# Performance work log

Hardware: AMD Instinct MI355X
Metric: run time of the kernel (lower is better)

## Reference

```python
import jax, jax.numpy as jnp
import numpy as np

NODE_DIM = 8
IN_EDGE_DIM = 4
OUT_EDGE_DIM = 4
HID = 16
N_NODES = 100000
N_EDGES = 3200000
LN_EPS = 1e-5


def _layer_norm(h, gamma, beta):
    mu = jnp.mean(h, axis=-1, keepdims=True)
    var = jnp.mean(jnp.square(h - mu), axis=-1, keepdims=True)
    return (h - mu) * jax.lax.rsqrt(var + LN_EPS) * gamma + beta


def setup_inputs() -> dict:
    key = jax.random.key(0)
    ks = jax.random.split(key, 12)
    in_dim = NODE_DIM * 2 + IN_EDGE_DIM  # 20
    x = jax.random.normal(ks[0], (N_NODES, NODE_DIM), dtype=jnp.float32)
    edge_index = jax.random.randint(ks[1], (2, N_EDGES), 0, N_NODES, dtype=jnp.int64)
    edge_attr = jax.random.normal(ks[2], (N_EDGES, IN_EDGE_DIM), dtype=jnp.float32)
    # MLP params (Kaiming-uniform-ish scaling like torch defaults)
    def lin(k, fan_in, fan_out):
        lim = 1.0 / np.sqrt(fan_in)
        kw, kb = jax.random.split(k)
        W = jax.random.uniform(kw, (fan_in, fan_out), minval=-lim, maxval=lim, dtype=jnp.float32)
        b = jax.random.uniform(kb, (fan_out,), minval=-lim, maxval=lim, dtype=jnp.float32)
        return W, b
    W1, b1 = lin(ks[3], in_dim, HID)
    W2, b2 = lin(ks[4], HID, HID)
    W3, b3 = lin(ks[5], HID, OUT_EDGE_DIM)
    g1 = jnp.ones((HID,), jnp.float32); be1 = jnp.zeros((HID,), jnp.float32)
    g2 = jnp.ones((HID,), jnp.float32); be2 = jnp.zeros((HID,), jnp.float32)
    return {"x": x, "edge_index": edge_index, "edge_attr": edge_attr,
            "W1": W1, "b1": b1, "g1": g1, "be1": be1,
            "W2": W2, "b2": b2, "g2": g2, "be2": be2,
            "W3": W3, "b3": b3}


def reference(x, edge_index, edge_attr, W1, b1, g1, be1, W2, b2, g2, be2, W3, b3):
    frm = edge_index[0]
    to = edge_index[1]
    # gather node features for both endpoints, concat with edge features: [E, 2*node_dim+in_edge_dim]
    inpt = jnp.concatenate([x[frm], x[to], edge_attr.astype(jnp.float32)], axis=1)
    h = _layer_norm(jax.nn.relu(inpt @ W1 + b1), g1, be1)
    h = _layer_norm(jax.nn.relu(h @ W2 + b2), g2, be2)
    return h @ W3 + b3  # [E, out_edge_dim]
```

## Files before the change

kernel.cpp:

```cpp
#include <hip/hip_runtime.h>
#include <stdint.h>


using u16 = unsigned short;
using u32 = uint32_t;
typedef float v2f __attribute__((ext_vector_type(2)));
typedef __attribute__((ext_vector_type(4))) float f32x4;
typedef __attribute__((ext_vector_type(8))) short bf16x8;
typedef __attribute__((ext_vector_type(2))) __bf16 bf16x2;

__device__ __forceinline__ v2f v2fma(v2f a, v2f b, v2f c) {
    return __builtin_elementwise_fma(a, b, c);
}
__device__ __forceinline__ v2f v2max0(v2f a) {
    v2f z = {0.f, 0.f};
    return __builtin_elementwise_max(a, z);
}

__device__ __forceinline__ float bf2f(u16 u) { return __uint_as_float(((u32)u) << 16); }
__device__ __forceinline__ float bflo(u32 u) { return __uint_as_float(u << 16); }
__device__ __forceinline__ float bfhi(u32 u) { return __uint_as_float(u & 0xFFFF0000u); }
__device__ __forceinline__ u32 f2bf(float f) {
    u32 u = __float_as_uint(f);
    return (u + 0x7FFFu + ((u >> 16) & 1u)) >> 16;
}
__device__ __forceinline__ u32 pkbf(float a, float b) {
    bf16x2 t;
    t.x = (__bf16)a;
    t.y = (__bf16)b;
    return __builtin_bit_cast(u32, t);
}
__device__ __forceinline__ float ldw(const void* p, int i, bool bf) {
    return bf ? bf2f(((const u16*)p)[i]) : ((const float*)p)[i];
}

#define WB_W1 0
#define WB_B1 320
#define WB_W2 336
#define WB_B2 592
#define WB_W3 608
#define WB_B3 672
#define WB_TOT 704
#define WV_W1 0
#define WV_B1 160
#define WV_W2 168
#define WV_B2 296
#define WV_W3 304
#define WV_B3 336
#define FQ_A1 0
#define FQ_A2H 512
#define FQ_A2L 1024
#define FQ_A3H 1536
#define FQ_A3L 2048
#define FB_OFF (WB_TOT + 1280)

__global__ __launch_bounds__(256)
void probe_convert(const int* __restrict__ ei, int n_pairs,
                   const void* W1, const void* b1, const void* g1, const void* be1,
                   const void* W2, const void* b2, const void* g2, const void* be2,
                   const void* W3, const void* b3,
                   int* __restrict__ flags, float* __restrict__ wb) {
    bool bf = (((const u32*)g1)[0] == 0x3F803F80u);
    __shared__ int s;
    if (threadIdx.x == 0) s = 0;
    __syncthreads();
    int limit = n_pairs < 2048 ? n_pairs : 2048;
    int found = 0;
    for (int i = threadIdx.x; i < limit; i += blockDim.x)
        if (ei[2 * i + 1] != 0) found = 1;
    if (found) s = 1;
    __syncthreads();
    if (threadIdx.x == 0) { flags[0] = s; flags[1] = bf ? 1 : 0; }

    int t = threadIdx.x;
    for (int i = t; i < 320; i += 256) wb[WB_W1 + i] = ldw(W1, i, bf);
    if (t < 16) wb[WB_B1 + t] = ldw(b1, t, bf);
    {
        int k = t >> 4;
        wb[WB_W2 + t] = ldw(g1, k, bf) * ldw(W2, t, bf);
    }
    if (t < 16) {
        float acc = ldw(b2, t, bf);
        for (int k = 0; k < 16; k++) acc = fmaf(ldw(be1, k, bf), ldw(W2, k * 16 + t, bf), acc);
        wb[WB_B2 + t] = acc;
    }
    if (t < 64) {
        int k = t >> 2;
        wb[WB_W3 + t] = ldw(g2, k, bf) * ldw(W3, t, bf);
    }
    if (t < 4) {
        float acc = ldw(b3, t, bf);
        for (int k = 0; k < 16; k++) acc = fmaf(ldw(be2, k, bf), ldw(W3, k * 4 + t, bf), acc);
        wb[WB_B3 + t] = acc;
    }
    if (t >= 4 && t < 32) wb[672 + t] = 0.f;

    __syncthreads();

    u16* fq = (u16*)(wb + WB_TOT);
    for (int i = t; i < 512; i += 256) {
        int l = i >> 3, j = i & 7;
        int m = l & 15, g = l >> 4;
        int k = g * 8 + j;
        int kk = k & 15;
        fq[FQ_A1 + i] = (u16)f2bf(k < 20 ? wb[WB_W1 + k * 16 + m] : 0.f);
        float w2 = wb[WB_W2 + kk * 16 + m];
        u16 h2 = (u16)f2bf(w2);
        fq[FQ_A2H + i] = h2;
        fq[FQ_A2L + i] = (u16)f2bf(w2 - bf2f(h2));
        float w3 = (m < 4) ? wb[WB_W3 + kk * 4 + m] : 0.f;
        u16 h3 = (u16)f2bf(w3);
        fq[FQ_A3H + i] = h3;
        fq[FQ_A3L + i] = (u16)f2bf(w3 - bf2f(h3));
    }
    {
        float* fbv = wb + FB_OFF;
        int l = t >> 2, r = t & 3;
        int row = ((l >> 4) << 2) + r;
        fbv[t] = wb[WB_B1 + row];
        fbv[256 + t] = wb[WB_B2 + row];
        fbv[512 + t] = (row < 4) ? wb[WB_B3 + row] : 0.f;
    }
}

__device__ __forceinline__ void ln16(f32x4 d, float& h0, float& h1, float& h2, float& h3) {
    f32x4 z = {0.f, 0.f, 0.f, 0.f};
    d = __builtin_elementwise_max(d, z);
    float s = (d.x + d.y) + (d.z + d.w);
    float q = fmaf(d.x, d.x, fmaf(d.y, d.y, fmaf(d.z, d.z, d.w * d.w)));
    s += __shfl_xor(s, 16);
    q += __shfl_xor(q, 16);
    s += __shfl_xor(s, 32);
    q += __shfl_xor(q, 32);
    float mu = s * 0.0625f;
    float var = fmaf(-mu, mu, q * 0.0625f);
    float r = rsqrtf(var + 1e-5f);
    float nb = -mu * r;
    h0 = fmaf(d.x, r, nb);
    h1 = fmaf(d.y, r, nb);
    h2 = fmaf(d.z, r, nb);
    h3 = fmaf(d.w, r, nb);
}

__device__ __forceinline__ bf16x8 redist_split(float h0, float h1, float h2, float h3,
                                               int n, int g) {
    u32 hi01 = pkbf(h0, h1), hi23 = pkbf(h2, h3);
    float r0 = h0 - bflo(hi01);
    float r1 = h1 - bfhi(hi01);
    float r2 = h2 - bflo(hi23);
    float r3 = h3 - bfhi(hi23);
    u32 lo01 = pkbf(r0, r1), lo23 = pkbf(r2, r3);
    int srcA = n + (((g & 1) << 1) << 4);
    int srcB = srcA + 16;
    u32 hA01 = (u32)__shfl((int)hi01, srcA);
    u32 hA23 = (u32)__shfl((int)hi23, srcA);
    u32 lA01 = (u32)__shfl((int)lo01, srcA);
    u32 lA23 = (u32)__shfl((int)lo23, srcA);
    u32 hB01 = (u32)__shfl((int)hi01, srcB);
    u32 hB23 = (u32)__shfl((int)hi23, srcB);
    u32 lB01 = (u32)__shfl((int)lo01, srcB);
    u32 lB23 = (u32)__shfl((int)lo23, srcB);
    bool hi = (g < 2);
    uint4 uu = make_uint4(hi ? hA01 : lA01, hi ? hA23 : lA23,
                          hi ? hB01 : lB01, hi ? hB23 : lB23);
    return __builtin_bit_cast(bf16x8, uu);
}

#define TPW 8

__global__ __launch_bounds__(256, 6)
void edge_mlp_mfma(const void* __restrict__ x, const int* __restrict__ ei,
                   const void* __restrict__ ea, const float* __restrict__ wb,
                   const int* __restrict__ flags, void* __restrict__ out, int n_edges) {
    if (flags[1] == 0) return;
    const bool idx32 = flags[0] != 0;

    const int lane = threadIdx.x & 63;
    const int n = lane & 15;
    const int g = lane >> 4;

    const u16* fq = (const u16*)(wb + WB_TOT);
    bf16x8 A1  = ((const bf16x8*)fq)[lane];
    bf16x8 A2h = ((const bf16x8*)fq)[64 + lane];
    bf16x8 A2l = ((const bf16x8*)fq)[128 + lane];
    bf16x8 A3h = ((const bf16x8*)fq)[192 + lane];
    bf16x8 A3l = ((const bf16x8*)fq)[256 + lane];
    const f32x4* fb = (const f32x4*)(wb + FB_OFF);
    f32x4 pb1 = fb[lane];
    f32x4 pb2 = fb[64 + lane];
    f32x4 pb3 = fb[128 + lane];

    const int ntiles = (n_edges + 15) >> 4;
    const int wflat = blockIdx.x * 4 + (threadIdx.x >> 6);
    const int t0 = wflat * TPW;

#pragma unroll 1
    for (int ti = 0; ti < TPW; ++ti) {
        int tile = t0 + ti;
        if (tile >= ntiles) break;

        int e = (tile << 4) + n;
        bool ev = e < n_edges;

        uint4 raw = make_uint4(0u, 0u, 0u, 0u);
        if (g < 2) {
            size_t col = (g == 0) ? (size_t)e : ((size_t)n_edges + (size_t)e);
            int idx = 0;
            if (ev) idx = idx32 ? ei[col] : ei[2 * col];
            raw = ((const uint4*)x)[idx];
        } else if (g == 2) {
            if (ev) {
                uint2 r = ((const uint2*)ea)[e];
                raw.x = r.x;
                raw.y = r.y;
            }
        }

        f32x4 d1 = pb1;
        d1 = __builtin_amdgcn_mfma_f32_16x16x32_bf16(A1, __builtin_bit_cast(bf16x8, raw),
                                                     d1, 0, 0, 0);
        float h0, h1, h2, h3;
        ln16(d1, h0, h1, h2, h3);

        bf16x8 f2 = redist_split(h0, h1, h2, h3, n, g);
        f32x4 d2 = pb2;
        d2 = __builtin_amdgcn_mfma_f32_16x16x32_bf16(A2h, f2, d2, 0, 0, 0);
        d2 = __builtin_amdgcn_mfma_f32_16x16x32_bf16(A2l, f2, d2, 0, 0, 0);
        float z0, z1, z2, z3;
        ln16(d2, z0, z1, z2, z3);

        bf16x8 f3 = redist_split(z0, z1, z2, z3, n, g);
        f32x4 d3 = pb3;
        d3 = __builtin_amdgcn_mfma_f32_16x16x32_bf16(A3h, f3, d3, 0, 0, 0);
        d3 = __builtin_amdgcn_mfma_f32_16x16x32_bf16(A3l, f3, d3, 0, 0, 0);

        if (g == 0 && ev) {
            u32 p0 = pkbf(d3.x, d3.y);
            u32 p1 = pkbf(d3.z, d3.w);
            ((uint2*)out)[e] = make_uint2(p0, p1);
        }
    }
}

__device__ __forceinline__ void relu_ln8v(v2f* h) {
    v2f sv = {0.f, 0.f}, qv = {0.f, 0.f};
#pragma unroll
    for (int p = 0; p < 8; p++) {
        h[p] = v2max0(h[p]);
        sv += h[p];
        qv = v2fma(h[p], h[p], qv);
    }
    float s = sv.x + sv.y, q = qv.x + qv.y;
    float mu = s * 0.0625f;
    float var = fmaf(-mu, mu, q * 0.0625f);
    float r = rsqrtf(var + 1e-5f);
    float n = -mu * r;
    v2f rv = {r, r}, nv = {n, n};
#pragma unroll
    for (int p = 0; p < 8; p++) h[p] = v2fma(h[p], rv, nv);
}

__device__ __forceinline__ void rows4(v2f* h, const v2f* __restrict__ wv,
                                      float4 v, int base) {
    float c[4] = {v.x, v.y, v.z, v.w};
#pragma unroll
    for (int t = 0; t < 4; t++) {
        const v2f* w = wv + WV_W1 + (base + t) * 8;
        v2f a = {c[t], c[t]};
#pragma unroll
        for (int p = 0; p < 8; p++) h[p] = v2fma(a, w[p], h[p]);
    }
}

__global__ __launch_bounds__(256)
void edge_mlp(const void* __restrict__ x, const int* __restrict__ ei,
              const void* __restrict__ ea, const float* __restrict__ wb,
              const int* __restrict__ flags, void* __restrict__ out, int n_edges) {
    if (flags[1] != 0) return;
    const v2f* wv = (const v2f*)wb;
    const bool idx32 = flags[0] != 0;

    int e = blockIdx.x * 256 + threadIdx.x;
    if (e >= n_edges) return;

    int frm, to;
    if (idx32) {
        frm = ei[e];
        to  = ei[n_edges + e];
    } else {
        frm = ei[2 * (size_t)e];
        to  = ei[2 * ((size_t)n_edges + e)];
    }

    v2f h[8];
#pragma unroll
    for (int p = 0; p < 8; p++) h[p] = wv[WV_B1 + p];

    const float4* xp = (const float4*)x;
    float4 xa = xp[2 * frm], xb = xp[2 * frm + 1];
    float4 xc = xp[2 * to],  xd = xp[2 * to + 1];
    float4 evv = ((const float4*)ea)[e];
    rows4(h, wv, xa, 0);
    rows4(h, wv, xb, 4);
    rows4(h, wv, xc, 8);
    rows4(h, wv, xd, 12);
    rows4(h, wv, evv, 16);

    relu_ln8v(h);

    v2f av[8];
#pragma unroll
    for (int p = 0; p < 8; p++) av[p] = wv[WV_B2 + p];
#pragma unroll
    for (int k = 0; k < 16; k++) {
        float z = (k & 1) ? h[k >> 1].y : h[k >> 1].x;
        v2f zb = {z, z};
        const v2f* w = wv + WV_W2 + k * 8;
#pragma unroll
        for (int p = 0; p < 8; p++) av[p] = v2fma(zb, w[p], av[p]);
    }

    relu_ln8v(av);

    v2f oa = wv[WV_B3 + 0], ob = wv[WV_B3 + 1];
#pragma unroll
    for (int k = 0; k < 16; k++) {
        float z = (k & 1) ? av[k >> 1].y : av[k >> 1].x;
        v2f zb = {z, z};
        oa = v2fma(zb, wv[WV_W3 + k * 2], oa);
        ob = v2fma(zb, wv[WV_W3 + k * 2 + 1], ob);
    }

    ((float4*)out)[e] = make_float4(oa.x, oa.y, ob.x, ob.y);
}

extern "C" void kernel_launch(void* const* d_in, const int* in_sizes, int n_in,
                              void* d_out, int out_size, void* d_ws, size_t ws_size,
                              hipStream_t stream) {
    const void* x  = d_in[0];
    const int* ei  = (const int*)d_in[1];
    const void* ea = d_in[2];

    int n_edges = in_sizes[1] / 2;

    int* flags = (int*)d_ws;
    float* wb = (float*)((char*)d_ws + 64);

    probe_convert<<<1, 256, 0, stream>>>(ei, n_edges,
                                         d_in[3], d_in[4], d_in[5], d_in[6],
                                         d_in[7], d_in[8], d_in[9], d_in[10],
                                         d_in[11], d_in[12], flags, wb);

    int ntiles = (n_edges + 15) / 16;
    int mblocks = (ntiles + 4 * TPW - 1) / (4 * TPW);
    edge_mlp_mfma<<<mblocks, 256, 0, stream>>>(x, ei, ea, wb, flags, d_out, n_edges);

    int eblocks = (n_edges + 255) / 256;
    edge_mlp<<<eblocks, 256, 0, stream>>>(x, ei, ea, wb, flags, d_out, n_edges);
}
```

Baseline: 205.2 us.

## Route the fp32 path through split-bf16 MFMA and drop the scalar kernel

The fp32 input path now runs through the MFMA kernel instead of the per-edge scalar FMA kernel. Layer-1 weights and fp32 gathered inputs are split into high and low bf16 parts and combined with three MFMAs, which approximates fp32 accuracy. The scalar kernel and its launch are removed, and the MFMA kernel writes fp32 output when inputs are fp32. The aim is to move the dense per-edge matmul work onto matrix cores, at the cost of extra conversion work, more registers (launch bounds lowered from 6 to 4 waves) and a slightly lower-precision approximation.

After: 214.4 us. +4.5%, slower.

```diff
diff --git a/kernel.cpp b/kernel.cpp
--- a/kernel.cpp
+++ b/kernel.cpp
@@ -4,18 +4,9 @@
 
 using u16 = unsigned short;
 using u32 = uint32_t;
-typedef float v2f __attribute__((ext_vector_type(2)));
 typedef __attribute__((ext_vector_type(4))) float f32x4;
 typedef __attribute__((ext_vector_type(8))) short bf16x8;
 typedef __attribute__((ext_vector_type(2))) __bf16 bf16x2;
-
-__device__ __forceinline__ v2f v2fma(v2f a, v2f b, v2f c) {
-    return __builtin_elementwise_fma(a, b, c);
-}
-__device__ __forceinline__ v2f v2max0(v2f a) {
-    v2f z = {0.f, 0.f};
-    return __builtin_elementwise_max(a, z);
-}
 
 __device__ __forceinline__ float bf2f(u16 u) { return __uint_as_float(((u32)u) << 16); }
 __device__ __forceinline__ float bflo(u32 u) { return __uint_as_float(u << 16); }
@@ -41,18 +32,13 @@
 #define WB_W3 608
 #define WB_B3 672
 #define WB_TOT 704
-#define WV_W1 0
-#define WV_B1 160
-#define WV_W2 168
-#define WV_B2 296
-#define WV_W3 304
-#define WV_B3 336
-#define FQ_A1 0
-#define FQ_A2H 512
-#define FQ_A2L 1024
-#define FQ_A3H 1536
-#define FQ_A3L 2048
-#define FB_OFF (WB_TOT + 1280)
+#define FQ_A1H 0
+#define FQ_A1L 512
+#define FQ_A2H 1024
+#define FQ_A2L 1536
+#define FQ_A3H 2048
+#define FQ_A3L 2560
+#define FB_OFF (WB_TOT + 1536)
 
 __global__ __launch_bounds__(256)
 void probe_convert(const int* __restrict__ ei, int n_pairs,
@@ -103,7 +89,10 @@
         int m = l & 15, g = l >> 4;
         int k = g * 8 + j;
         int kk = k & 15;
-        fq[FQ_A1 + i] = (u16)f2bf(k < 20 ? wb[WB_W1 + k * 16 + m] : 0.f);
+        float w1 = (k < 20) ? wb[WB_W1 + k * 16 + m] : 0.f;
+        u16 h1 = (u16)f2bf(w1);
+        fq[FQ_A1H + i] = h1;
+        fq[FQ_A1L + i] = (u16)f2bf(w1 - bf2f(h1));
         float w2 = wb[WB_W2 + kk * 16 + m];
         u16 h2 = (u16)f2bf(w2);
         fq[FQ_A2H + i] = h2;
@@ -168,23 +157,24 @@
 
 #define TPW 8
 
-__global__ __launch_bounds__(256, 6)
+__global__ __launch_bounds__(256, 4)
 void edge_mlp_mfma(const void* __restrict__ x, const int* __restrict__ ei,
                    const void* __restrict__ ea, const float* __restrict__ wb,
                    const int* __restrict__ flags, void* __restrict__ out, int n_edges) {
-    if (flags[1] == 0) return;
     const bool idx32 = flags[0] != 0;
+    const bool bf = flags[1] != 0;
 
     const int lane = threadIdx.x & 63;
     const int n = lane & 15;
     const int g = lane >> 4;
 
     const u16* fq = (const u16*)(wb + WB_TOT);
-    bf16x8 A1  = ((const bf16x8*)fq)[lane];
-    bf16x8 A2h = ((const bf16x8*)fq)[64 + lane];
-    bf16x8 A2l = ((const bf16x8*)fq)[128 + lane];
-    bf16x8 A3h = ((const bf16x8*)fq)[192 + lane];
-    bf16x8 A3l = ((const bf16x8*)fq)[256 + lane];
+    bf16x8 A1h = ((const bf16x8*)fq)[0 * 64 + lane];
+    bf16x8 A1l = ((const bf16x8*)fq)[1 * 64 + lane];
+    bf16x8 A2h = ((const bf16x8*)fq)[2 * 64 + lane];
+    bf16x8 A2l = ((const bf16x8*)fq)[3 * 64 + lane];
+    bf16x8 A3h = ((const bf16x8*)fq)[4 * 64 + lane];
+    bf16x8 A3l = ((const bf16x8*)fq)[5 * 64 + lane];
     const f32x4* fb = (const f32x4*)(wb + FB_OFF);
     f32x4 pb1 = fb[lane];
     f32x4 pb2 = fb[64 + lane];
@@ -202,136 +192,74 @@
         int e = (tile << 4) + n;
         bool ev = e < n_edges;
 
-        uint4 raw = make_uint4(0u, 0u, 0u, 0u);
-        if (g < 2) {
+        int idx = 0;
+        if (g < 2 && ev) {
             size_t col = (g == 0) ? (size_t)e : ((size_t)n_edges + (size_t)e);
-            int idx = 0;
-            if (ev) idx = idx32 ? ei[col] : ei[2 * col];
-            raw = ((const uint4*)x)[idx];
-        } else if (g == 2) {
-            if (ev) {
+            idx = idx32 ? ei[col] : ei[2 * col];
+        }
+
+        f32x4 d1 = pb1;
+        if (bf) {
+            uint4 raw = make_uint4(0u, 0u, 0u, 0u);
+            if (g < 2) {
+                raw = ((const uint4*)x)[idx];
+            } else if (g == 2 && ev) {
                 uint2 r = ((const uint2*)ea)[e];
                 raw.x = r.x;
                 raw.y = r.y;
             }
+            d1 = __builtin_amdgcn_mfma_f32_16x16x32_bf16(
+                A1h, __builtin_bit_cast(bf16x8, raw), d1, 0, 0, 0);
+        } else {
+            float f0 = 0.f, f1 = 0.f, f2 = 0.f, f3 = 0.f;
+            float f4 = 0.f, f5 = 0.f, f6 = 0.f, f7 = 0.f;
+            if (g < 2) {
+                const float4* xp = (const float4*)x;
+                float4 a = xp[2 * idx], b = xp[2 * idx + 1];
+                f0 = a.x; f1 = a.y; f2 = a.z; f3 = a.w;
+                f4 = b.x; f5 = b.y; f6 = b.z; f7 = b.w;
+            } else if (g == 2 && ev) {
+                float4 r = ((const float4*)ea)[e];
+                f0 = r.x; f1 = r.y; f2 = r.z; f3 = r.w;
+            }
+            u32 h01 = pkbf(f0, f1), h23 = pkbf(f2, f3);
+            u32 h45 = pkbf(f4, f5), h67 = pkbf(f6, f7);
+            u32 l01 = pkbf(f0 - bflo(h01), f1 - bfhi(h01));
+            u32 l23 = pkbf(f2 - bflo(h23), f3 - bfhi(h23));
+            u32 l45 = pkbf(f4 - bflo(h45), f5 - bfhi(h45));
+            u32 l67 = pkbf(f6 - bflo(h67), f7 - bfhi(h67));
+            bf16x8 Bh = __builtin_bit_cast(bf16x8, make_uint4(h01, h23, h45, h67));
+            bf16x8 Bl = __builtin_bit_cast(bf16x8, make_uint4(l01, l23, l45, l67));
+            d1 = __builtin_amdgcn_mfma_f32_16x16x32_bf16(A1h, Bh, d1, 0, 0, 0);
+            d1 = __builtin_amdgcn_mfma_f32_16x16x32_bf16(A1h, Bl, d1, 0, 0, 0);
+            d1 = __builtin_amdgcn_mfma_f32_16x16x32_bf16(A1l, Bh, d1, 0, 0, 0);
         }
 
-        f32x4 d1 = pb1;
-        d1 = __builtin_amdgcn_mfma_f32_16x16x32_bf16(A1, __builtin_bit_cast(bf16x8, raw),
-                                                     d1, 0, 0, 0);
         float h0, h1, h2, h3;
         ln16(d1, h0, h1, h2, h3);
 
-        bf16x8 f2 = redist_split(h0, h1, h2, h3, n, g);
+        bf16x8 f2v = redist_split(h0, h1, h2, h3, n, g);
         f32x4 d2 = pb2;
-        d2 = __builtin_amdgcn_mfma_f32_16x16x32_bf16(A2h, f2, d2, 0, 0, 0);
-        d2 = __builtin_amdgcn_mfma_f32_16x16x32_bf16(A2l, f2, d2, 0, 0, 0);
+        d2 = __builtin_amdgcn_mfma_f32_16x16x32_bf16(A2h, f2v, d2, 0, 0, 0);
+        d2 = __builtin_amdgcn_mfma_f32_16x16x32_bf16(A2l, f2v, d2, 0, 0, 0);
         float z0, z1, z2, z3;
         ln16(d2, z0, z1, z2, z3);
 
-        bf16x8 f3 = redist_split(z0, z1, z2, z3, n, g);
+        bf16x8 f3v = redist_split(z0, z1, z2, z3, n, g);
         f32x4 d3 = pb3;
-        d3 = __builtin_amdgcn_mfma_f32_16x16x32_bf16(A3h, f3, d3, 0, 0, 0);
-        d3 = __builtin_amdgcn_mfma_f32_16x16x32_bf16(A3l, f3, d3, 0, 0, 0);
+        d3 = __builtin_amdgcn_mfma_f32_16x16x32_bf16(A3h, f3v, d3, 0, 0, 0);
+        d3 = __builtin_amdgcn_mfma_f32_16x16x32_bf16(A3l, f3v, d3, 0, 0, 0);
 
         if (g == 0 && ev) {
-            u32 p0 = pkbf(d3.x, d3.y);
-            u32 p1 = pkbf(d3.z, d3.w);
-            ((uint2*)out)[e] = make_uint2(p0, p1);
+            if (bf) {
+                u32 p0 = pkbf(d3.x, d3.y);
+                u32 p1 = pkbf(d3.z, d3.w);
+                ((uint2*)out)[e] = make_uint2(p0, p1);
+            } else {
+                ((float4*)out)[e] = make_float4(d3.x, d3.y, d3.z, d3.w);
+            }
         }
     }
-}
-
-__device__ __forceinline__ void relu_ln8v(v2f* h) {
-    v2f sv = {0.f, 0.f}, qv = {0.f, 0.f};
-#pragma unroll
-    for (int p = 0; p < 8; p++) {
-        h[p] = v2max0(h[p]);
-        sv += h[p];
-        qv = v2fma(h[p], h[p], qv);
-    }
-    float s = sv.x + sv.y, q = qv.x + qv.y;
-    float mu = s * 0.0625f;
-    float var = fmaf(-mu, mu, q * 0.0625f);
-    float r = rsqrtf(var + 1e-5f);
-    float n = -mu * r;
-    v2f rv = {r, r}, nv = {n, n};
-#pragma unroll
-    for (int p = 0; p < 8; p++) h[p] = v2fma(h[p], rv, nv);
-}
-
-__device__ __forceinline__ void rows4(v2f* h, const v2f* __restrict__ wv,
-                                      float4 v, int base) {
-    float c[4] = {v.x, v.y, v.z, v.w};
-#pragma unroll
-    for (int t = 0; t < 4; t++) {
-        const v2f* w = wv + WV_W1 + (base + t) * 8;
-        v2f a = {c[t], c[t]};
-#pragma unroll
-        for (int p = 0; p < 8; p++) h[p] = v2fma(a, w[p], h[p]);
-    }
-}
-
-__global__ __launch_bounds__(256)
-void edge_mlp(const void* __restrict__ x, const int* __restrict__ ei,
-              const void* __restrict__ ea, const float* __restrict__ wb,
-              const int* __restrict__ flags, void* __restrict__ out, int n_edges) {
-    if (flags[1] != 0) return;
-    const v2f* wv = (const v2f*)wb;
-    const bool idx32 = flags[0] != 0;
-
-    int e = blockIdx.x * 256 + threadIdx.x;
-    if (e >= n_edges) return;
-
-    int frm, to;
-    if (idx32) {
-        frm = ei[e];
-        to  = ei[n_edges + e];
-    } else {
-        frm = ei[2 * (size_t)e];
-        to  = ei[2 * ((size_t)n_edges + e)];
-    }
-
-    v2f h[8];
-#pragma unroll
-    for (int p = 0; p < 8; p++) h[p] = wv[WV_B1 + p];
-
-    const float4* xp = (const float4*)x;
-    float4 xa = xp[2 * frm], xb = xp[2 * frm + 1];
-    float4 xc = xp[2 * to],  xd = xp[2 * to + 1];
-    float4 evv = ((const float4*)ea)[e];
-    rows4(h, wv, xa, 0);
-    rows4(h, wv, xb, 4);
-    rows4(h, wv, xc, 8);
-    rows4(h, wv, xd, 12);
-    rows4(h, wv, evv, 16);
-
-    relu_ln8v(h);
-
-    v2f av[8];
-#pragma unroll
-    for (int p = 0; p < 8; p++) av[p] = wv[WV_B2 + p];
-#pragma unroll
-    for (int k = 0; k < 16; k++) {
-        float z = (k & 1) ? h[k >> 1].y : h[k >> 1].x;
-        v2f zb = {z, z};
-        const v2f* w = wv + WV_W2 + k * 8;
-#pragma unroll
-        for (int p = 0; p < 8; p++) av[p] = v2fma(zb, w[p], av[p]);
-    }
-
-    relu_ln8v(av);
-
-    v2f oa = wv[WV_B3 + 0], ob = wv[WV_B3 + 1];
-#pragma unroll
-    for (int k = 0; k < 16; k++) {
-        float z = (k & 1) ? av[k >> 1].y : av[k >> 1].x;
-        v2f zb = {z, z};
-        oa = v2fma(zb, wv[WV_W3 + k * 2], oa);
-        ob = v2fma(zb, wv[WV_W3 + k * 2 + 1], ob);
-    }
-
-    ((float4*)out)[e] = make_float4(oa.x, oa.y, ob.x, ob.y);
 }
 
 extern "C" void kernel_launch(void* const* d_in, const int* in_sizes, int n_in,
@@ -354,7 +282,4 @@
     int ntiles = (n_edges + 15) / 16;
     int mblocks = (ntiles + 4 * TPW - 1) / (4 * TPW);
     edge_mlp_mfma<<<mblocks, 256, 0, stream>>>(x, ei, ea, wb, flags, d_out, n_edges);
-
-    int eblocks = (n_edges + 255) / 256;
-    edge_mlp<<<eblocks, 256, 0, stream>>>(x, ei, ea, wb, flags, d_out, n_edges);
-}
+}
```
